# Kernel optimization log

Measured on AMD Instinct MI355X. Metric: run time of the kernel, lower is better.

Reference implementation:

```python
import jax, jax.numpy as jnp
import numpy as np
from jax import lax

H = 768            # encoder hidden size (bert-base)
NUM_LABELS = 3     # hardcoded in QNetwork.forward


def setup_inputs() -> dict:
    key = jax.random.key(0)
    ks = jax.random.split(key, 12)
    B, S1, S2 = 4, 256, 64
    s = 0.02
    f32 = jnp.float32
    return {
        "states": jax.random.normal(ks[0], (B, S1, H), f32),
        "state_mask": jnp.ones((B, S1), f32),
        "actions": jax.random.normal(ks[1], (B, S2, H), f32),
        "actions_mask": jnp.ones((B, S2), f32),
        # LSTM layer 0 (input h), layers 1-2 (input 2h); dirs stacked on axis 0
        "Wih0": jax.random.normal(ks[2], (2, 4 * H, H), f32) * s,
        "Whh0": jax.random.normal(ks[3], (2, 4 * H, H), f32) * s,
        "b0": jnp.zeros((2, 4 * H), f32),
        "Wih12": jax.random.normal(ks[4], (2, 2, 4 * H, 2 * H), f32) * s,
        "Whh12": jax.random.normal(ks[5], (2, 2, 4 * H, H), f32) * s,
        "b12": jnp.zeros((2, 2, 4 * H), f32),
        # AttentionLayer MLP: Linear(3h->h), ReLU, Linear(h->1)
        "attn_W1": jax.random.normal(ks[6], (H, 3 * H), f32) * s,
        "attn_b1": jnp.zeros((H,), f32),
        "attn_W2": jax.random.normal(ks[7], (1, H), f32) * s,
        "attn_b2": jnp.zeros((1,), f32),
        # dueling value head Linear(2h->1)
        "val_W": jax.random.normal(ks[8], (1, 2 * H), f32) * s,
        "val_b": jnp.zeros((1,), f32),
        # bilinear scoring weight [num_labels, h, 2h] and bias [num_labels]
        "weight": jax.random.normal(ks[9], (NUM_LABELS, H, 2 * H), f32) * s,
        "bias": jnp.zeros((NUM_LABELS,), f32),
    }


def _bilstm_layer(x, Wih, Whh, b):
    """x: [B,T,in]; Wih/Whh: [2,4h,*]; b: [2,4h] (b_ih+b_hh). Returns [B,T,2h]."""
    B = x.shape[0]
    Hh = Whh.shape[-1]
    xs = jnp.swapaxes(x, 0, 1)  # [T,B,in]
    outs = []
    for d, rev in ((0, False), (1, True)):
        Wi, Wh, bb = Wih[d], Whh[d], b[d]
        def step(carry, xt, Wi=Wi, Wh=Wh, bb=bb):
            h, c = carry
            g = xt @ Wi.T + h @ Wh.T + bb
            i, f, gg, o = jnp.split(g, 4, axis=-1)  # torch gate order i,f,g,o
            c = jax.nn.sigmoid(f) * c + jax.nn.sigmoid(i) * jnp.tanh(gg)
            h = jax.nn.sigmoid(o) * jnp.tanh(c)
            return (h, c), h
        init = (jnp.zeros((B, Hh), x.dtype), jnp.zeros((B, Hh), x.dtype))
        _, ys = lax.scan(step, init, xs, reverse=rev)
        outs.append(jnp.swapaxes(ys, 0, 1))
    return jnp.concatenate(outs, -1)


def _forward(states, state_mask, actions, actions_mask,
             Wih0, Whh0, b0, Wih12, Whh12, b12,
             attn_W1, attn_b1, attn_W2, attn_b2,
             val_W, val_b, weight, bias):
    # 3-layer bidirectional LSTM + tanh
    out = _bilstm_layer(states, Wih0, Whh0, b0)
    for l in range(2):
        out = _bilstm_layer(out, Wih12[l], Whh12[l], b12[l])
    out = jnp.tanh(out)  # [B,S1,2h]

    # AttentionLayer(query=actions, key=value=out, q_mask=actions_mask, k_mask=state_mask)
    # First linear on concat([q,k]) split into query/key parts to avoid materializing the 3h concat.
    W1q, W1k = attn_W1[:, :H], attn_W1[:, H:]
    hq = jnp.einsum('bqh,eh->bqe', actions, W1q)          # [B,S2,h]
    hk = jnp.einsum('bkh,eh->bke', out, W1k)              # [B,S1,h]
    h1 = jax.nn.relu(hq[:, :, None, :] + hk[:, None, :, :] + attn_b1)  # [B,S2,S1,h]
    scores = jnp.einsum('bqke,e->bqk', h1, attn_W2[0]) + attn_b2[0]    # [B,S2,S1]
    mask = actions_mask[:, :, None] * state_mask[:, None, :]
    A = jnp.exp(jnp.where(mask == 0, -jnp.inf, scores))
    A_sum = jnp.clip(jnp.sum(A, axis=-1, keepdims=True), 2e-15, None)
    states_feat = jnp.einsum('bqk,bkd->bqd', A / A_sum, out)  # [B,S2,2h]

    # masked mean over seq2 (aggregate='attn_mean')
    num = jnp.sum(actions_mask, axis=1)[:, None, None]
    state_semantic = jnp.sum(states_feat, axis=1, keepdims=True) / num  # [B,1,2h]

    # adv scores: sum_h actions[b,q,h] * (weight[l,h,d] states_feat[b,q,d])
    adv = jnp.einsum('lhd,bqd,bqh->bql', weight, states_feat, actions) + bias  # [B,S2,3]

    # dueling value head
    val = state_semantic @ val_W.T + val_b  # [B,1,1]
    q_value = val + adv - jnp.mean(adv, axis=(1, 2), keepdims=True)  # [B,S2,3]

    # actions_mask is all-ones so the nonzero-gather is the identity
    return q_value.reshape(-1, NUM_LABELS)


def reference(states, state_mask, actions, actions_mask,
              Wih0, Whh0, b0, Wih12, Whh12, b12,
              attn_W1, attn_b1, attn_W2, attn_b2,
              val_W, val_b, weight, bias):
    return _forward(states, state_mask, actions, actions_mask,
                    Wih0, Whh0, b0, Wih12, Whh12, b12,
                    attn_W1, attn_b1, attn_W2, attn_b2,
                    val_W, val_b, weight, bias)
```

## Files before the change

kernel.cpp:

```cpp
#include <hip/hip_runtime.h>

#define HD 768
#define G4 3072
#define T1 256
#define NS2 64
#define NL 3
#define NBLK_DIR 128
#define UPB 6

__device__ __forceinline__ float sigf(float x) { return 1.0f / (1.0f + expf(-x)); }

__device__ __forceinline__ void fence_vm() {
    asm volatile("s_waitcnt vmcnt(0)" ::: "memory");
}

__global__ __launch_bounds__(256) void gemm_f32(
    const float* __restrict__ A, int lda,
    const float* __restrict__ W, int ldw,
    const float* __restrict__ bias,
    float* __restrict__ C,
    int K, int n_per_chunk, long long chunk_stride)
{
    __shared__ __align__(16) float As[16 * 64];
    __shared__ __align__(16) float Ws[16 * 64];
    const int tid = threadIdx.x;
    const int tx = tid & 15, ty = tid >> 4;
    const int n0 = blockIdx.x * 64, m0 = blockIdx.y * 64;
    const int lr = tid >> 2, lc = tid & 3;

    float acc[4][4] = {{0.f}};
    const float* Ap = A + (size_t)(m0 + lr) * lda + lc * 4;
    const float* Wp = W + (size_t)(n0 + lr) * ldw + lc * 4;

    for (int k0 = 0; k0 < K; k0 += 16) {
        float4 av = *(const float4*)(Ap + k0);
        float4 wv = *(const float4*)(Wp + k0);
        __syncthreads();
        As[(lc * 4 + 0) * 64 + lr] = av.x;
        As[(lc * 4 + 1) * 64 + lr] = av.y;
        As[(lc * 4 + 2) * 64 + lr] = av.z;
        As[(lc * 4 + 3) * 64 + lr] = av.w;
        Ws[(lc * 4 + 0) * 64 + lr] = wv.x;
        Ws[(lc * 4 + 1) * 64 + lr] = wv.y;
        Ws[(lc * 4 + 2) * 64 + lr] = wv.z;
        Ws[(lc * 4 + 3) * 64 + lr] = wv.w;
        __syncthreads();
#pragma unroll
        for (int k = 0; k < 16; ++k) {
            float4 a = *(const float4*)&As[k * 64 + ty * 4];
            float4 b = *(const float4*)&Ws[k * 64 + tx * 4];
            float aa[4] = {a.x, a.y, a.z, a.w};
            float bb[4] = {b.x, b.y, b.z, b.w};
#pragma unroll
            for (int i = 0; i < 4; ++i)
#pragma unroll
                for (int j = 0; j < 4; ++j) acc[i][j] += aa[i] * bb[j];
        }
    }

    const int jg = n0 + tx * 4;
    const int chunk = jg / n_per_chunk;
    const int jo = jg - chunk * n_per_chunk;
    float4 bv = make_float4(0.f, 0.f, 0.f, 0.f);
    if (bias) bv = *(const float4*)&bias[jg];
    float* Cb = C + (size_t)chunk * chunk_stride + jo;
#pragma unroll
    for (int i = 0; i < 4; ++i) {
        const int m = m0 + ty * 4 + i;
        float4 o;
        o.x = acc[i][0] + bv.x;
        o.y = acc[i][1] + bv.y;
        o.z = acc[i][2] + bv.z;
        o.w = acc[i][3] + bv.w;
        *(float4*)&Cb[(size_t)m * n_per_chunk] = o;
    }
}

__global__ __launch_bounds__(256) void lstm_scan(
    const float* __restrict__ Whh,
    const float* __restrict__ G,
    float* __restrict__ Hout,
    float* __restrict__ hglob,
    unsigned* __restrict__ bar,
    int last)
{
    __shared__ __align__(16) float4 hs[960];
    __shared__ float gl[24 * 4];
    __shared__ float cst[24];
    const int tid = threadIdx.x;
    const int bid = blockIdx.x;
    const int dir = bid & 1;
    const int blkd = bid >> 1;
    const int u0 = blkd * UPB;

    const int ks = tid & 15, jp = tid >> 4;
    const bool act = (jp < 12);
    const bool kz = act && (ks == 0);

    const int r0 = 2 * jp, r1 = 2 * jp + 1;
    const int j0 = (r0 / 6) * HD + u0 + (r0 % 6);
    const int j1 = (r1 / 6) * HD + u0 + (r1 % 6);
    float4 w0[12], w1[12];
    if (act) {
        const float4* W4 = (const float4*)Whh + (size_t)dir * G4 * 192;
#pragma unroll
        for (int i = 0; i < 12; ++i) {
            w0[i] = W4[(size_t)j0 * 192 + i * 16 + ks];
            w1[i] = W4[(size_t)j1 * 192 + i * 16 + ks];
        }
    }
    if (tid < 24) cst[tid] = 0.f;

    unsigned* ctr = bar + dir * 256;
    unsigned* genp = bar + 512 + dir * 32;
    const size_t gdb = (size_t)dir * 4 * T1 * G4;
    const size_t bstr = (size_t)T1 * G4;
    float* hsf = (float*)hs;

    for (int s = 0; s < T1; ++s) {
        const int t = dir ? (T1 - 1 - s) : s;

        float gA[4], gB[4];
        if (kz) {
            const float* Gt = G + gdb + (size_t)t * G4;
#pragma unroll
            for (int b = 0; b < 4; ++b) {
                gA[b] = Gt[(size_t)b * bstr + j0];
                gB[b] = Gt[(size_t)b * bstr + j1];
            }
        }

        if (s == 0) {
#pragma unroll
            for (int r = 0; r < 3; ++r) {
                const int k = tid + 256 * r;
                hs[5 * (k >> 2) + (k & 3)] = make_float4(0.f, 0.f, 0.f, 0.f);
            }
        } else {
            const float* hp = hglob + ((size_t)((s & 1) * 2 + dir)) * HD * 4;
            float hv[12];
#pragma unroll
            for (int r = 0; r < 12; ++r)
                hv[r] = __hip_atomic_load(hp + tid + 256 * r, __ATOMIC_RELAXED,
                                          __HIP_MEMORY_SCOPE_AGENT);
#pragma unroll
            for (int r = 0; r < 12; ++r) {
                const int i = tid + 256 * r;
                const int k = i >> 2, b = i & 3;
                hsf[(5 * (k >> 2) + (k & 3)) * 4 + b] = hv[r];
            }
        }
        __syncthreads();

        if (act) {
            float4 a0 = make_float4(0.f, 0.f, 0.f, 0.f);
            float4 a1 = make_float4(0.f, 0.f, 0.f, 0.f);
#pragma unroll
            for (int i = 0; i < 12; ++i) {
                const int pb = 5 * (i * 16 + ks);
                const float4 h0 = hs[pb + 0];
                const float4 h1 = hs[pb + 1];
                const float4 h2 = hs[pb + 2];
                const float4 h3 = hs[pb + 3];
                const float4 wa = w0[i];
                const float4 wb = w1[i];
                a0.x += wa.x * h0.x; a0.y += wa.x * h0.y; a0.z += wa.x * h0.z; a0.w += wa.x * h0.w;
                a0.x += wa.y * h1.x; a0.y += wa.y * h1.y; a0.z += wa.y * h1.z; a0.w += wa.y * h1.w;
                a0.x += wa.z * h2.x; a0.y += wa.z * h2.y; a0.z += wa.z * h2.z; a0.w += wa.z * h2.w;
                a0.x += wa.w * h3.x; a0.y += wa.w * h3.y; a0.z += wa.w * h3.z; a0.w += wa.w * h3.w;
                a1.x += wb.x * h0.x; a1.y += wb.x * h0.y; a1.z += wb.x * h0.z; a1.w += wb.x * h0.w;
                a1.x += wb.y * h1.x; a1.y += wb.y * h1.y; a1.z += wb.y * h1.z; a1.w += wb.y * h1.w;
                a1.x += wb.z * h2.x; a1.y += wb.z * h2.y; a1.z += wb.z * h2.z; a1.w += wb.z * h2.w;
                a1.x += wb.w * h3.x; a1.y += wb.w * h3.y; a1.z += wb.w * h3.z; a1.w += wb.w * h3.w;
            }
#pragma unroll
            for (int off = 8; off; off >>= 1) {
                a0.x += __shfl_xor(a0.x, off);
                a0.y += __shfl_xor(a0.y, off);
                a0.z += __shfl_xor(a0.z, off);
                a0.w += __shfl_xor(a0.w, off);
                a1.x += __shfl_xor(a1.x, off);
                a1.y += __shfl_xor(a1.y, off);
                a1.z += __shfl_xor(a1.z, off);
                a1.w += __shfl_xor(a1.w, off);
            }
            if (ks == 0) {
                gl[r0 * 4 + 0] = a0.x + gA[0];
                gl[r0 * 4 + 1] = a0.y + gA[1];
                gl[r0 * 4 + 2] = a0.z + gA[2];
                gl[r0 * 4 + 3] = a0.w + gA[3];
                gl[r1 * 4 + 0] = a1.x + gB[0];
                gl[r1 * 4 + 1] = a1.y + gB[1];
                gl[r1 * 4 + 2] = a1.z + gB[2];
                gl[r1 * 4 + 3] = a1.w + gB[3];
            }
        }
        __syncthreads();

        if (tid < 24) {
            const int ui = tid >> 2, b = tid & 3;
            const float gi = gl[(0 * 6 + ui) * 4 + b];
            const float gf = gl[(1 * 6 + ui) * 4 + b];
            const float gg = gl[(2 * 6 + ui) * 4 + b];
            const float go = gl[(3 * 6 + ui) * 4 + b];
            const float c = sigf(gf) * cst[tid] + sigf(gi) * tanhf(gg);
            const float h = sigf(go) * tanhf(c);
            cst[tid] = c;
            __hip_atomic_store(
                &hglob[(((size_t)(((s + 1) & 1) * 2 + dir)) * HD + (u0 + ui)) * 4 + b],
                h, __ATOMIC_RELAXED, __HIP_MEMORY_SCOPE_AGENT);
            Hout[((size_t)b * T1 + t) * (2 * HD) + dir * HD + (u0 + ui)] =
                last ? tanhf(h) : h;
            fence_vm();
        }

        if (s < T1 - 1) {
            __syncthreads();
            if (tid == 0) {
                __hip_atomic_fetch_add(&ctr[(blkd & 7) * 32], 1u, __ATOMIC_RELAXED,
                                       __HIP_MEMORY_SCOPE_AGENT);
                const unsigned tgt = (unsigned)(NBLK_DIR * (s + 1));
                if (blkd == 0) {
                    for (;;) {
                        unsigned sum = 0;
#pragma unroll
                        for (int i = 0; i < 8; ++i)
                            sum += __hip_atomic_load(&ctr[i * 32], __ATOMIC_RELAXED,
                                                     __HIP_MEMORY_SCOPE_AGENT);
                        if (sum >= tgt) break;
                    }
                    __hip_atomic_store(genp, (unsigned)(s + 1), __ATOMIC_RELAXED,
                                       __HIP_MEMORY_SCOPE_AGENT);
                } else {
                    while (__hip_atomic_load(genp, __ATOMIC_RELAXED,
                                             __HIP_MEMORY_SCOPE_AGENT) <
                           (unsigned)(s + 1)) {}
                }
            }
            __syncthreads();
        }
    }
}

__global__ __launch_bounds__(256) void attn_kernel(
    const float* __restrict__ hq,
    const float* __restrict__ hk,
    const float* __restrict__ w2p,
    const float* __restrict__ b2p,
    const float* __restrict__ am,
    const float* __restrict__ sm,
    const float* __restrict__ H3,
    float* __restrict__ sf)
{
    __shared__ float hql[HD];
    __shared__ float w2[HD];
    __shared__ float Ash[T1];
    __shared__ float red[1];
    const int tid = threadIdx.x;
    const int bq = blockIdx.x;
    const int b = bq >> 6;

    for (int e = tid; e < HD; e += 256) {
        hql[e] = hq[(size_t)bq * HD + e];
        w2[e] = w2p[e];
    }
    __syncthreads();

    const int lane = tid & 63, wid = tid >> 6;
    const float amv = am[bq];
    const float b2 = b2p[0];
    for (int k = wid; k < T1; k += 4) {
        const float* hkp = hk + ((size_t)b * T1 + k) * HD;
        float s = 0.f;
#pragma unroll
        for (int i = 0; i < 12; ++i) {
            const int e = i * 64 + lane;
            float v = hql[e] + hkp[e];
            v = v > 0.f ? v : 0.f;
            s += v * w2[e];
        }
#pragma unroll
        for (int off = 32; off; off >>= 1) s += __shfl_xor(s, off);
        if (lane == 0) {
            const float m = amv * sm[b * T1 + k];
            Ash[k] = (m == 0.f) ? 0.f : expf(s + b2);
        }
    }
    __syncthreads();

    if (tid < 64) {
        float p = Ash[tid] + Ash[tid + 64] + Ash[tid + 128] + Ash[tid + 192];
#pragma unroll
        for (int off = 32; off; off >>= 1) p += __shfl_xor(p, off);
        if (tid == 0) red[0] = fmaxf(p, 2e-15f);
    }
    __syncthreads();
    const float inv = 1.f / red[0];

    for (int d = tid; d < 2 * HD; d += 256) {
        const float* hp = H3 + (size_t)b * T1 * 2 * HD + d;
        float acc = 0.f;
        for (int k = 0; k < T1; ++k) acc += Ash[k] * hp[(size_t)k * 2 * HD];
        sf[(size_t)bq * 2 * HD + d] = acc * inv;
    }
}

__global__ __launch_bounds__(256) void val_kernel(
    const float* __restrict__ sf, const float* __restrict__ am,
    const float* __restrict__ vw, const float* __restrict__ vb,
    float* __restrict__ val)
{
    __shared__ float red[4];
    const int b = blockIdx.x, tid = threadIdx.x;
    float num = 0.f;
    for (int q = 0; q < NS2; ++q) num += am[b * NS2 + q];
    float acc = 0.f;
    for (int d = tid; d < 2 * HD; d += 256) {
        float s = 0.f;
        for (int q = 0; q < NS2; ++q) s += sf[((size_t)(b * NS2 + q)) * 2 * HD + d];
        acc += (s / num) * vw[d];
    }
#pragma unroll
    for (int off = 32; off; off >>= 1) acc += __shfl_xor(acc, off);
    if ((tid & 63) == 0) red[tid >> 6] = acc;
    __syncthreads();
    if (tid == 0) val[b] = red[0] + red[1] + red[2] + red[3] + vb[0];
}

__global__ __launch_bounds__(256) void final_kernel(
    const float* __restrict__ Tb,
    const float* __restrict__ act,
    const float* __restrict__ bias,
    const float* __restrict__ val,
    float* __restrict__ out)
{
    __shared__ float adv[192];
    __shared__ float red[4];
    const int b = blockIdx.x, tid = threadIdx.x;
    const int lane = tid & 63, wid = tid >> 6;

    for (int idx = wid; idx < 192; idx += 4) {
        const int q = idx / 3, l = idx - q * 3;
        const float* tp = Tb + (size_t)l * T1 * HD + (size_t)(b * NS2 + q) * HD;
        const float* ap = act + (size_t)(b * NS2 + q) * HD;
        float s = 0.f;
#pragma unroll
        for (int i = 0; i < 12; ++i) {
            const int h = i * 64 + lane;
            s += tp[h] * ap[h];
        }
#pragma unroll
        for (int off = 32; off; off >>= 1) s += __shfl_xor(s, off);
        if (lane == 0) adv[idx] = s + bias[l];
    }
    __syncthreads();
    float part = (tid < 192) ? adv[tid] : 0.f;
#pragma unroll
    for (int off = 32; off; off >>= 1) part += __shfl_xor(part, off);
    if (lane == 0) red[wid] = part;
    __syncthreads();
    const float mean = (red[0] + red[1] + red[2] + red[3]) * (1.f / 192.f);
    const float vv = val[b];
    for (int idx = tid; idx < 192; idx += 256) {
        const int q = idx / 3, l = idx - q * 3;
        out[(size_t)(b * NS2 + q) * NL + l] = vv + adv[idx] - mean;
    }
}

extern "C" void kernel_launch(void* const* d_in, const int* in_sizes, int n_in,
                              void* d_out, int out_size, void* d_ws, size_t ws_size,
                              hipStream_t stream)
{
    const float* states = (const float*)d_in[0];
    const float* state_mask = (const float*)d_in[1];
    const float* actions = (const float*)d_in[2];
    const float* actions_mask = (const float*)d_in[3];
    const float* Wih0 = (const float*)d_in[4];
    const float* Whh0 = (const float*)d_in[5];
    const float* b0 = (const float*)d_in[6];
    const float* Wih12 = (const float*)d_in[7];
    const float* Whh12 = (const float*)d_in[8];
    const float* b12 = (const float*)d_in[9];
    const float* aW1 = (const float*)d_in[10];
    const float* ab1 = (const float*)d_in[11];
    const float* aW2 = (const float*)d_in[12];
    const float* ab2 = (const float*)d_in[13];
    const float* vW = (const float*)d_in[14];
    const float* vb = (const float*)d_in[15];
    const float* wgt = (const float*)d_in[16];
    const float* bias = (const float*)d_in[17];
    float* out = (float*)d_out;

    float* ws = (float*)d_ws;
    float* G = ws;
    float* B1 = G + 6291456;
    float* B2 = B1 + 1572864;
    float* hg = B2 + 1572864;
    unsigned* bar = (unsigned*)(hg + 12288);
    float* hq = G;
    float* hkb = G + 196608;
    float* sf = G + 983040;
    float* Tb = G + 1376256;
    float* val = G + 1966080;

    const dim3 blk(256);
    const long long gstride = (long long)4 * T1 * G4;

    hipMemsetAsync(bar, 0, 4096, stream);
    gemm_f32<<<dim3(6144 / 64, 1024 / 64), blk, 0, stream>>>(
        states, HD, Wih0, HD, b0, G, HD, G4, gstride);
    lstm_scan<<<dim3(256), blk, 0, stream>>>(Whh0, G, B1, hg, bar, 0);
    hipMemsetAsync(bar, 0, 4096, stream);
    gemm_f32<<<dim3(6144 / 64, 1024 / 64), blk, 0, stream>>>(
        B1, 2 * HD, Wih12, 2 * HD, b12, G, 2 * HD, G4, gstride);
    lstm_scan<<<dim3(256), blk, 0, stream>>>(Whh12, G, B2, hg, bar, 0);
    hipMemsetAsync(bar, 0, 4096, stream);
    gemm_f32<<<dim3(6144 / 64, 1024 / 64), blk, 0, stream>>>(
        B2, 2 * HD, Wih12 + (size_t)6144 * 1536, 2 * HD, b12 + 6144, G, 2 * HD, G4, gstride);
    lstm_scan<<<dim3(256), blk, 0, stream>>>(
        Whh12 + (size_t)2 * G4 * HD, G, B1, hg, bar, 1);
    gemm_f32<<<dim3(768 / 64, 256 / 64), blk, 0, stream>>>(
        actions, HD, aW1, 2304, ab1, hq, HD, HD, 0);
    gemm_f32<<<dim3(768 / 64, 1024 / 64), blk, 0, stream>>>(
        B1, 2 * HD, aW1 + 768, 2304, nullptr, hkb, 2 * HD, HD, 0);
    attn_kernel<<<dim3(256), blk, 0, stream>>>(hq, hkb, aW2, ab2, actions_mask,
                                               state_mask, B1, sf);
    val_kernel<<<dim3(4), blk, 0, stream>>>(sf, actions_mask, vW, vb, val);
    for (int l = 0; l < NL; ++l) {
        gemm_f32<<<dim3(768 / 64, 256 / 64), blk, 0, stream>>>(
            sf, 2 * HD, wgt + (size_t)l * HD * 2 * HD, 2 * HD, nullptr,
            Tb + (size_t)l * T1 * HD, 2 * HD, HD, 0);
    }
    final_kernel<<<dim3(4), blk, 0, stream>>>(Tb, actions, bias, val, out);
}
```

Before: 4.280 ms.

## Use 128x128 GEMM tiles and a decentralized grid barrier in LSTM scan

The GEMM tile grows from 64x64 to 128x128, with 8x8 accumulators per thread for more register reuse. The LSTM scan barrier drops the leader block and its generation flag: every block polls the eight counters with a wavefront of eight lanes and sums them with shuffles. The counter increment now happens right after the h store fence. The next step's input gates are prefetched before the barrier wait, to shorten the serial critical path of the 256-step recurrence. Larger tiles cut the block count to very few for the small GEMMs (12 blocks), and all blocks polling the shared counters adds contention.

Result: slower. 4.910 ms (+14.7%).

```diff
diff --git a/kernel.cpp b/kernel.cpp
--- a/kernel.cpp
+++ b/kernel.cpp
@@ -21,58 +21,74 @@
     float* __restrict__ C,
     int K, int n_per_chunk, long long chunk_stride)
 {
-    __shared__ __align__(16) float As[16 * 64];
-    __shared__ __align__(16) float Ws[16 * 64];
+    __shared__ __align__(16) float As[16 * 128];
+    __shared__ __align__(16) float Ws[16 * 128];
     const int tid = threadIdx.x;
     const int tx = tid & 15, ty = tid >> 4;
-    const int n0 = blockIdx.x * 64, m0 = blockIdx.y * 64;
-    const int lr = tid >> 2, lc = tid & 3;
-
-    float acc[4][4] = {{0.f}};
-    const float* Ap = A + (size_t)(m0 + lr) * lda + lc * 4;
-    const float* Wp = W + (size_t)(n0 + lr) * ldw + lc * 4;
+    const int n0 = blockIdx.x * 128, m0 = blockIdx.y * 128;
+    const int lr = tid >> 1, lc = tid & 1;
+
+    float acc[8][8] = {{0.f}};
+    const float* Ap = A + (size_t)(m0 + lr) * lda + lc * 8;
+    const float* Wp = W + (size_t)(n0 + lr) * ldw + lc * 8;
 
     for (int k0 = 0; k0 < K; k0 += 16) {
-        float4 av = *(const float4*)(Ap + k0);
-        float4 wv = *(const float4*)(Wp + k0);
+        float4 a0 = *(const float4*)(Ap + k0);
+        float4 a1 = *(const float4*)(Ap + k0 + 4);
+        float4 b0 = *(const float4*)(Wp + k0);
+        float4 b1 = *(const float4*)(Wp + k0 + 4);
         __syncthreads();
-        As[(lc * 4 + 0) * 64 + lr] = av.x;
-        As[(lc * 4 + 1) * 64 + lr] = av.y;
-        As[(lc * 4 + 2) * 64 + lr] = av.z;
-        As[(lc * 4 + 3) * 64 + lr] = av.w;
-        Ws[(lc * 4 + 0) * 64 + lr] = wv.x;
-        Ws[(lc * 4 + 1) * 64 + lr] = wv.y;
-        Ws[(lc * 4 + 2) * 64 + lr] = wv.z;
-        Ws[(lc * 4 + 3) * 64 + lr] = wv.w;
+        const int kb = lc * 8;
+        As[(kb + 0) * 128 + lr] = a0.x;
+        As[(kb + 1) * 128 + lr] = a0.y;
+        As[(kb + 2) * 128 + lr] = a0.z;
+        As[(kb + 3) * 128 + lr] = a0.w;
+        As[(kb + 4) * 128 + lr] = a1.x;
+        As[(kb + 5) * 128 + lr] = a1.y;
+        As[(kb + 6) * 128 + lr] = a1.z;
+        As[(kb + 7) * 128 + lr] = a1.w;
+        Ws[(kb + 0) * 128 + lr] = b0.x;
+        Ws[(kb + 1) * 128 + lr] = b0.y;
+        Ws[(kb + 2) * 128 + lr] = b0.z;
+        Ws[(kb + 3) * 128 + lr] = b0.w;
+        Ws[(kb + 4) * 128 + lr] = b1.x;
+        Ws[(kb + 5) * 128 + lr] = b1.y;
+        Ws[(kb + 6) * 128 + lr] = b1.z;
+        Ws[(kb + 7) * 128 + lr] = b1.w;
         __syncthreads();
 #pragma unroll
         for (int k = 0; k < 16; ++k) {
-            float4 a = *(const float4*)&As[k * 64 + ty * 4];
-            float4 b = *(const float4*)&Ws[k * 64 + tx * 4];
-            float aa[4] = {a.x, a.y, a.z, a.w};
-            float bb[4] = {b.x, b.y, b.z, b.w};
-#pragma unroll
-            for (int i = 0; i < 4; ++i)
-#pragma unroll
-                for (int j = 0; j < 4; ++j) acc[i][j] += aa[i] * bb[j];
-        }
-    }
-
-    const int jg = n0 + tx * 4;
-    const int chunk = jg / n_per_chunk;
-    const int jo = jg - chunk * n_per_chunk;
-    float4 bv = make_float4(0.f, 0.f, 0.f, 0.f);
-    if (bias) bv = *(const float4*)&bias[jg];
-    float* Cb = C + (size_t)chunk * chunk_stride + jo;
-#pragma unroll
-    for (int i = 0; i < 4; ++i) {
-        const int m = m0 + ty * 4 + i;
-        float4 o;
-        o.x = acc[i][0] + bv.x;
-        o.y = acc[i][1] + bv.y;
-        o.z = acc[i][2] + bv.z;
-        o.w = acc[i][3] + bv.w;
-        *(float4*)&Cb[(size_t)m * n_per_chunk] = o;
+            float4 xa = *(const float4*)&As[k * 128 + ty * 4];
+            float4 xb = *(const float4*)&As[k * 128 + 64 + ty * 4];
+            float4 ya = *(const float4*)&Ws[k * 128 + tx * 4];
+            float4 yb = *(const float4*)&Ws[k * 128 + 64 + tx * 4];
+            float av[8] = {xa.x, xa.y, xa.z, xa.w, xb.x, xb.y, xb.z, xb.w};
+            float bv[8] = {ya.x, ya.y, ya.z, ya.w, yb.x, yb.y, yb.z, yb.w};
+#pragma unroll
+            for (int i = 0; i < 8; ++i)
+#pragma unroll
+                for (int j = 0; j < 8; ++j) acc[i][j] += av[i] * bv[j];
+        }
+    }
+
+#pragma unroll
+    for (int half = 0; half < 2; ++half) {
+        const int jg = n0 + half * 64 + tx * 4;
+        const int chunk = jg / n_per_chunk;
+        const int jo = jg - chunk * n_per_chunk;
+        float4 bv4 = make_float4(0.f, 0.f, 0.f, 0.f);
+        if (bias) bv4 = *(const float4*)&bias[jg];
+        float* Cb = C + (size_t)chunk * chunk_stride + jo;
+#pragma unroll
+        for (int i = 0; i < 8; ++i) {
+            const int m = m0 + (i < 4 ? ty * 4 + i : 64 + ty * 4 + (i - 4));
+            float4 o;
+            o.x = acc[i][half * 4 + 0] + bv4.x;
+            o.y = acc[i][half * 4 + 1] + bv4.y;
+            o.z = acc[i][half * 4 + 2] + bv4.z;
+            o.w = acc[i][half * 4 + 3] + bv4.w;
+            *(float4*)&Cb[(size_t)m * n_per_chunk] = o;
+        }
     }
 }
 
@@ -112,23 +128,23 @@
     if (tid < 24) cst[tid] = 0.f;
 
     unsigned* ctr = bar + dir * 256;
-    unsigned* genp = bar + 512 + dir * 32;
     const size_t gdb = (size_t)dir * 4 * T1 * G4;
     const size_t bstr = (size_t)T1 * G4;
     float* hsf = (float*)hs;
 
+    float gA[4], gB[4];
+    if (kz) {
+        const int t0 = dir ? (T1 - 1) : 0;
+        const float* Gt = G + gdb + (size_t)t0 * G4;
+#pragma unroll
+        for (int b = 0; b < 4; ++b) {
+            gA[b] = Gt[(size_t)b * bstr + j0];
+            gB[b] = Gt[(size_t)b * bstr + j1];
+        }
+    }
+
     for (int s = 0; s < T1; ++s) {
         const int t = dir ? (T1 - 1 - s) : s;
-
-        float gA[4], gB[4];
-        if (kz) {
-            const float* Gt = G + gdb + (size_t)t * G4;
-#pragma unroll
-            for (int b = 0; b < 4; ++b) {
-                gA[b] = Gt[(size_t)b * bstr + j0];
-                gB[b] = Gt[(size_t)b * bstr + j1];
-            }
-        }
 
         if (s == 0) {
 #pragma unroll
@@ -197,6 +213,7 @@
         }
         __syncthreads();
 
+        float hval = 0.f;
         if (tid < 24) {
             const int ui = tid >> 2, b = tid & 3;
             const float gi = gl[(0 * 6 + ui) * 4 + b];
@@ -204,38 +221,43 @@
             const float gg = gl[(2 * 6 + ui) * 4 + b];
             const float go = gl[(3 * 6 + ui) * 4 + b];
             const float c = sigf(gf) * cst[tid] + sigf(gi) * tanhf(gg);
-            const float h = sigf(go) * tanhf(c);
+            hval = sigf(go) * tanhf(c);
             cst[tid] = c;
             __hip_atomic_store(
                 &hglob[(((size_t)(((s + 1) & 1) * 2 + dir)) * HD + (u0 + ui)) * 4 + b],
-                h, __ATOMIC_RELAXED, __HIP_MEMORY_SCOPE_AGENT);
+                hval, __ATOMIC_RELAXED, __HIP_MEMORY_SCOPE_AGENT);
+        }
+        if (tid < 64) fence_vm();
+        if (s < T1 - 1 && tid == 0) {
+            __hip_atomic_fetch_add(&ctr[(blkd & 7) * 32], 1u, __ATOMIC_RELAXED,
+                                   __HIP_MEMORY_SCOPE_AGENT);
+        }
+        if (tid < 24) {
+            const int ui = tid >> 2, b = tid & 3;
             Hout[((size_t)b * T1 + t) * (2 * HD) + dir * HD + (u0 + ui)] =
-                last ? tanhf(h) : h;
-            fence_vm();
+                last ? tanhf(hval) : hval;
         }
 
         if (s < T1 - 1) {
-            __syncthreads();
-            if (tid == 0) {
-                __hip_atomic_fetch_add(&ctr[(blkd & 7) * 32], 1u, __ATOMIC_RELAXED,
-                                       __HIP_MEMORY_SCOPE_AGENT);
+            if (kz) {
+                const int tn = dir ? (T1 - 2 - s) : (s + 1);
+                const float* Gt = G + gdb + (size_t)tn * G4;
+#pragma unroll
+                for (int b = 0; b < 4; ++b) {
+                    gA[b] = Gt[(size_t)b * bstr + j0];
+                    gB[b] = Gt[(size_t)b * bstr + j1];
+                }
+            }
+            if (tid >= 192 && tid < 200) {
                 const unsigned tgt = (unsigned)(NBLK_DIR * (s + 1));
-                if (blkd == 0) {
-                    for (;;) {
-                        unsigned sum = 0;
-#pragma unroll
-                        for (int i = 0; i < 8; ++i)
-                            sum += __hip_atomic_load(&ctr[i * 32], __ATOMIC_RELAXED,
-                                                     __HIP_MEMORY_SCOPE_AGENT);
-                        if (sum >= tgt) break;
-                    }
-                    __hip_atomic_store(genp, (unsigned)(s + 1), __ATOMIC_RELAXED,
-                                       __HIP_MEMORY_SCOPE_AGENT);
-                } else {
-                    while (__hip_atomic_load(genp, __ATOMIC_RELAXED,
-                                             __HIP_MEMORY_SCOPE_AGENT) <
-                           (unsigned)(s + 1)) {}
-                }
+                unsigned sum;
+                do {
+                    sum = __hip_atomic_load(&ctr[(tid - 192) * 32], __ATOMIC_RELAXED,
+                                            __HIP_MEMORY_SCOPE_AGENT);
+                    sum += __shfl_xor(sum, 1, 8);
+                    sum += __shfl_xor(sum, 2, 8);
+                    sum += __shfl_xor(sum, 4, 8);
+                } while (sum < tgt);
             }
             __syncthreads();
         }
@@ -406,28 +428,28 @@
     const dim3 blk(256);
     const long long gstride = (long long)4 * T1 * G4;
 
-    hipMemsetAsync(bar, 0, 4096, stream);
-    gemm_f32<<<dim3(6144 / 64, 1024 / 64), blk, 0, stream>>>(
+    hipMemsetAsync(bar, 0, 2048, stream);
+    gemm_f32<<<dim3(6144 / 128, 1024 / 128), blk, 0, stream>>>(
         states, HD, Wih0, HD, b0, G, HD, G4, gstride);
     lstm_scan<<<dim3(256), blk, 0, stream>>>(Whh0, G, B1, hg, bar, 0);
-    hipMemsetAsync(bar, 0, 4096, stream);
-    gemm_f32<<<dim3(6144 / 64, 1024 / 64), blk, 0, stream>>>(
+    hipMemsetAsync(bar, 0, 2048, stream);
+    gemm_f32<<<dim3(6144 / 128, 1024 / 128), blk, 0, stream>>>(
         B1, 2 * HD, Wih12, 2 * HD, b12, G, 2 * HD, G4, gstride);
     lstm_scan<<<dim3(256), blk, 0, stream>>>(Whh12, G, B2, hg, bar, 0);
-    hipMemsetAsync(bar, 0, 4096, stream);
-    gemm_f32<<<dim3(6144 / 64, 1024 / 64), blk, 0, stream>>>(
+    hipMemsetAsync(bar, 0, 2048, stream);
+    gemm_f32<<<dim3(6144 / 128, 1024 / 128), blk, 0, stream>>>(
         B2, 2 * HD, Wih12 + (size_t)6144 * 1536, 2 * HD, b12 + 6144, G, 2 * HD, G4, gstride);
     lstm_scan<<<dim3(256), blk, 0, stream>>>(
         Whh12 + (size_t)2 * G4 * HD, G, B1, hg, bar, 1);
-    gemm_f32<<<dim3(768 / 64, 256 / 64), blk, 0, stream>>>(
+    gemm_f32<<<dim3(768 / 128, 256 / 128), blk, 0, stream>>>(
         actions, HD, aW1, 2304, ab1, hq, HD, HD, 0);
-    gemm_f32<<<dim3(768 / 64, 1024 / 64), blk, 0, stream>>>(
+    gemm_f32<<<dim3(768 / 128, 1024 / 128), blk, 0, stream>>>(
         B1, 2 * HD, aW1 + 768, 2304, nullptr, hkb, 2 * HD, HD, 0);
     attn_kernel<<<dim3(256), blk, 0, stream>>>(hq, hkb, aW2, ab2, actions_mask,
                                                state_mask, B1, sf);
     val_kernel<<<dim3(4), blk, 0, stream>>>(sf, actions_mask, vW, vb, val);
     for (int l = 0; l < NL; ++l) {
-        gemm_f32<<<dim3(768 / 64, 256 / 64), blk, 0, stream>>>(
+        gemm_f32<<<dim3(768 / 128, 256 / 128), blk, 0, stream>>>(
             sf, 2 * HD, wgt + (size_t)l * HD * 2 * HD, 2 * HD, nullptr,
             Tb + (size_t)l * T1 * HD, 2 * HD, HD, 0);
     }
```

## Use 128-row GEMM tiles, trim LSTM barrier sync, merge bilinear GEMMs

Applied to the files above, without the earlier changes.

Adds a gemm_f32_big kernel with 128x64 tiles (8x4 per thread) for the three LSTM input-projection GEMMs, raising arithmetic intensity per load. In the recurrent scan, the post-cell __syncthreads is dropped and the barrier counter increment is issued right after the h stores are fenced, before the Hout write. The shuffle reduction order is also flipped. The three per-label bilinear GEMMs are merged into one launch using the chunk stride. The scan's sequential barrier dominates runtime, so the fence/arrive reordering is the most consequential change, and it carries a risk of memory-ordering races.

Result: faster. 3.877 ms (-9.4%).

```diff
diff --git a/kernel.cpp b/kernel.cpp
--- a/kernel.cpp
+++ b/kernel.cpp
@@ -72,6 +72,76 @@
         o.y = acc[i][1] + bv.y;
         o.z = acc[i][2] + bv.z;
         o.w = acc[i][3] + bv.w;
+        *(float4*)&Cb[(size_t)m * n_per_chunk] = o;
+    }
+}
+
+__global__ __launch_bounds__(256) void gemm_f32_big(
+    const float* __restrict__ A, int lda,
+    const float* __restrict__ W, int ldw,
+    const float* __restrict__ bias,
+    float* __restrict__ C,
+    int K, int n_per_chunk, long long chunk_stride)
+{
+    __shared__ __align__(16) float As[16 * 128];
+    __shared__ __align__(16) float Ws[16 * 64];
+    const int tid = threadIdx.x;
+    const int tx = tid & 15, ty = tid >> 4;
+    const int n0 = blockIdx.x * 64, m0 = blockIdx.y * 128;
+    const int ar = tid >> 1, ac = tid & 1;
+    const int br = tid >> 2, bc = tid & 3;
+
+    float acc[8][4] = {{0.f}};
+    const float* Ap = A + (size_t)(m0 + ar) * lda + ac * 8;
+    const float* Wp = W + (size_t)(n0 + br) * ldw + bc * 4;
+
+    for (int k0 = 0; k0 < K; k0 += 16) {
+        float4 a0 = *(const float4*)(Ap + k0);
+        float4 a1 = *(const float4*)(Ap + k0 + 4);
+        float4 wv = *(const float4*)(Wp + k0);
+        __syncthreads();
+        const int kb = ac * 8;
+        As[(kb + 0) * 128 + ar] = a0.x;
+        As[(kb + 1) * 128 + ar] = a0.y;
+        As[(kb + 2) * 128 + ar] = a0.z;
+        As[(kb + 3) * 128 + ar] = a0.w;
+        As[(kb + 4) * 128 + ar] = a1.x;
+        As[(kb + 5) * 128 + ar] = a1.y;
+        As[(kb + 6) * 128 + ar] = a1.z;
+        As[(kb + 7) * 128 + ar] = a1.w;
+        Ws[(bc * 4 + 0) * 64 + br] = wv.x;
+        Ws[(bc * 4 + 1) * 64 + br] = wv.y;
+        Ws[(bc * 4 + 2) * 64 + br] = wv.z;
+        Ws[(bc * 4 + 3) * 64 + br] = wv.w;
+        __syncthreads();
+#pragma unroll
+        for (int k = 0; k < 16; ++k) {
+            float4 xa = *(const float4*)&As[k * 128 + ty * 8];
+            float4 xb = *(const float4*)&As[k * 128 + ty * 8 + 4];
+            float4 yv = *(const float4*)&Ws[k * 64 + tx * 4];
+            float av[8] = {xa.x, xa.y, xa.z, xa.w, xb.x, xb.y, xb.z, xb.w};
+            float bv[4] = {yv.x, yv.y, yv.z, yv.w};
+#pragma unroll
+            for (int i = 0; i < 8; ++i)
+#pragma unroll
+                for (int j = 0; j < 4; ++j) acc[i][j] += av[i] * bv[j];
+        }
+    }
+
+    const int jg = n0 + tx * 4;
+    const int chunk = jg / n_per_chunk;
+    const int jo = jg - chunk * n_per_chunk;
+    float4 bv4 = make_float4(0.f, 0.f, 0.f, 0.f);
+    if (bias) bv4 = *(const float4*)&bias[jg];
+    float* Cb = C + (size_t)chunk * chunk_stride + jo;
+#pragma unroll
+    for (int i = 0; i < 8; ++i) {
+        const int m = m0 + ty * 8 + i;
+        float4 o;
+        o.x = acc[i][0] + bv4.x;
+        o.y = acc[i][1] + bv4.y;
+        o.z = acc[i][2] + bv4.z;
+        o.w = acc[i][3] + bv4.w;
         *(float4*)&Cb[(size_t)m * n_per_chunk] = o;
     }
 }
@@ -174,7 +244,7 @@
                 a1.x += wb.w * h3.x; a1.y += wb.w * h3.y; a1.z += wb.w * h3.z; a1.w += wb.w * h3.w;
             }
 #pragma unroll
-            for (int off = 8; off; off >>= 1) {
+            for (int off = 1; off < 16; off <<= 1) {
                 a0.x += __shfl_xor(a0.x, off);
                 a0.y += __shfl_xor(a0.y, off);
                 a0.z += __shfl_xor(a0.z, off);
@@ -197,6 +267,7 @@
         }
         __syncthreads();
 
+        float hval = 0.f;
         if (tid < 24) {
             const int ui = tid >> 2, b = tid & 3;
             const float gi = gl[(0 * 6 + ui) * 4 + b];
@@ -204,21 +275,25 @@
             const float gg = gl[(2 * 6 + ui) * 4 + b];
             const float go = gl[(3 * 6 + ui) * 4 + b];
             const float c = sigf(gf) * cst[tid] + sigf(gi) * tanhf(gg);
-            const float h = sigf(go) * tanhf(c);
+            hval = sigf(go) * tanhf(c);
             cst[tid] = c;
             __hip_atomic_store(
                 &hglob[(((size_t)(((s + 1) & 1) * 2 + dir)) * HD + (u0 + ui)) * 4 + b],
-                h, __ATOMIC_RELAXED, __HIP_MEMORY_SCOPE_AGENT);
+                hval, __ATOMIC_RELAXED, __HIP_MEMORY_SCOPE_AGENT);
+        }
+        if (tid < 64) fence_vm();
+        if (s < T1 - 1 && tid == 0) {
+            __hip_atomic_fetch_add(&ctr[(blkd & 7) * 32], 1u, __ATOMIC_RELAXED,
+                                   __HIP_MEMORY_SCOPE_AGENT);
+        }
+        if (tid < 24) {
+            const int ui = tid >> 2, b = tid & 3;
             Hout[((size_t)b * T1 + t) * (2 * HD) + dir * HD + (u0 + ui)] =
-                last ? tanhf(h) : h;
-            fence_vm();
+                last ? tanhf(hval) : hval;
         }
 
         if (s < T1 - 1) {
-            __syncthreads();
             if (tid == 0) {
-                __hip_atomic_fetch_add(&ctr[(blkd & 7) * 32], 1u, __ATOMIC_RELAXED,
-                                       __HIP_MEMORY_SCOPE_AGENT);
                 const unsigned tgt = (unsigned)(NBLK_DIR * (s + 1));
                 if (blkd == 0) {
                     for (;;) {
@@ -407,15 +482,15 @@
     const long long gstride = (long long)4 * T1 * G4;
 
     hipMemsetAsync(bar, 0, 4096, stream);
-    gemm_f32<<<dim3(6144 / 64, 1024 / 64), blk, 0, stream>>>(
+    gemm_f32_big<<<dim3(6144 / 64, 1024 / 128), blk, 0, stream>>>(
         states, HD, Wih0, HD, b0, G, HD, G4, gstride);
     lstm_scan<<<dim3(256), blk, 0, stream>>>(Whh0, G, B1, hg, bar, 0);
     hipMemsetAsync(bar, 0, 4096, stream);
-    gemm_f32<<<dim3(6144 / 64, 1024 / 64), blk, 0, stream>>>(
+    gemm_f32_big<<<dim3(6144 / 64, 1024 / 128), blk, 0, stream>>>(
         B1, 2 * HD, Wih12, 2 * HD, b12, G, 2 * HD, G4, gstride);
     lstm_scan<<<dim3(256), blk, 0, stream>>>(Whh12, G, B2, hg, bar, 0);
     hipMemsetAsync(bar, 0, 4096, stream);
-    gemm_f32<<<dim3(6144 / 64, 1024 / 64), blk, 0, stream>>>(
+    gemm_f32_big<<<dim3(6144 / 64, 1024 / 128), blk, 0, stream>>>(
         B2, 2 * HD, Wih12 + (size_t)6144 * 1536, 2 * HD, b12 + 6144, G, 2 * HD, G4, gstride);
     lstm_scan<<<dim3(256), blk, 0, stream>>>(
         Whh12 + (size_t)2 * G4 * HD, G, B1, hg, bar, 1);
@@ -426,10 +501,7 @@
     attn_kernel<<<dim3(256), blk, 0, stream>>>(hq, hkb, aW2, ab2, actions_mask,
                                                state_mask, B1, sf);
     val_kernel<<<dim3(4), blk, 0, stream>>>(sf, actions_mask, vW, vb, val);
-    for (int l = 0; l < NL; ++l) {
-        gemm_f32<<<dim3(768 / 64, 256 / 64), blk, 0, stream>>>(
-            sf, 2 * HD, wgt + (size_t)l * HD * 2 * HD, 2 * HD, nullptr,
-            Tb + (size_t)l * T1 * HD, 2 * HD, HD, 0);
-    }
+    gemm_f32<<<dim3(2304 / 64, 256 / 64), blk, 0, stream>>>(
+        sf, 2 * HD, wgt, 2 * HD, nullptr, Tb, 2 * HD, HD, (long long)T1 * HD);
     final_kernel<<<dim3(4), blk, 0, stream>>>(Tb, actions, bias, val, out);
 }
```
